# Kernel optimization log

Measured on AMD Instinct MI355X. Metric: run time of the kernel, lower is better.

Reference implementation:

```python
import jax, jax.numpy as jnp
import numpy as np

D_OUT = 32
INPUT_LEN = 2048
NUM_EIGH = 32
K_U = 3
K_Y = 2


def _top_hankel_eigh(n, k):
    # Hankel matrix Z[i,j] = 2 / ((i+j)^3 - (i+j)) for i,j in 1..n
    i = np.arange(1, n + 1, dtype=np.float64)
    s = i[:, None] + i[None, :]
    Z = 2.0 / (s ** 3 - s)
    vals, vecs = np.linalg.eigh(Z)
    return (jnp.asarray(vals[-k:], dtype=jnp.float32),
            jnp.asarray(vecs[:, -k:], dtype=jnp.float32))


def setup_inputs() -> dict:
    key = jax.random.key(0)
    k1, k2, k3, k4 = jax.random.split(key, 4)
    B = 32
    inputs = jax.random.normal(k1, (B, INPUT_LEN, D_OUT), dtype=jnp.float32)
    eig_vals, eig_vecs = _top_hankel_eigh(INPUT_LEN, NUM_EIGH)
    m_u = jax.random.normal(k2, (D_OUT, D_OUT, K_U), dtype=jnp.float32) * 0.02
    m_phi = jax.random.normal(k3, (D_OUT * NUM_EIGH, D_OUT), dtype=jnp.float32) * 0.02
    m_y = jax.random.normal(k4, (D_OUT, K_Y, D_OUT), dtype=jnp.float32) * 0.02
    return {"inputs": inputs, "eig_vals": eig_vals, "eig_vecs": eig_vecs,
            "m_u": m_u, "m_phi": m_phi, "m_y": m_y}


def _spectral_conv(v, u):
    # Causal FFT convolution of each filter v[:,k] with each channel u[:,:,d].
    # v: (l, k), u: (b, l, d) -> (b, l, k, d)
    l = v.shape[0]
    n = 2 * l
    V = jnp.fft.rfft(v, n=n, axis=0)          # (nf, k)
    U = jnp.fft.rfft(u, n=n, axis=1)          # (b, nf, d)
    P = V[None, :, :, None] * U[:, :, None, :]  # (b, nf, k, d)
    return jnp.fft.irfft(P, n=n, axis=1)[:, :l]


def _compute_x_tilde(inputs, eig_vals, eig_vecs):
    b, l, d = inputs.shape
    x_tilde = _spectral_conv(eig_vecs, inputs)                  # (b, l, k, d)
    x_tilde = x_tilde * (eig_vals ** 0.25)[None, None, :, None]
    return x_tilde.reshape(b, l, -1)                            # (b, l, k*d)


def _compute_ar_x_preds(w, x):
    # w: (d_out, d_in, k), x: (b, l, d_in) -> (b, l, d_out)
    d_out, d_in, k = w.shape
    b, l, _ = x.shape
    o = jnp.einsum('oik,bli->bklo', w, x)                       # (b, k, l, d_out)
    shifts = jnp.arange(k)
    rolled = jax.vmap(lambda oi, s: jnp.roll(oi, s, axis=1),
                      in_axes=(1, 0), out_axes=1)(o, shifts)    # (b, k, l, d_out)
    mask = (jnp.arange(l)[None, :] >= shifts[:, None]).astype(x.dtype)  # (k, l)
    return jnp.sum(rolled * mask[None, :, :, None], axis=1)


def _compute_y_t(m_y, deltas):
    # m_y: (d_out, k_y, d_out), deltas: (b, l, d_out)
    # y_t = sum_{j<k_y} m_y[:, j] @ y_{t-1-j} + delta_t
    b, l, d = deltas.shape
    ky = m_y.shape[1]
    carry0 = jnp.zeros((b, ky, d), dtype=deltas.dtype)

    def step(carry, x):
        out = jnp.einsum('oki,bki->bo', m_y, carry) + x
        carry = jnp.roll(carry, 1, axis=1).at[:, 0].set(out)
        return carry, out

    _, ys = jax.lax.scan(step, carry0, jnp.swapaxes(deltas, 0, 1))
    return jnp.swapaxes(ys, 0, 1)


def reference(inputs, eig_vals, eig_vecs, m_u, m_phi, m_y):
    x_tilde = _compute_x_tilde(inputs, eig_vals, eig_vecs)
    delta_phi = x_tilde @ m_phi
    delta_ar_u = _compute_ar_x_preds(m_u, inputs)
    return _compute_y_t(m_y, delta_phi + delta_ar_u)
```

## Files before the change

kernel.cpp:

```cpp
#include <hip/hip_runtime.h>
#include <math.h>

#define L     2048
#define NFFT  4096
#define NH    2049
#define UST   2052
#define D     32
#define B     32
#define KU    3
#define CCH   64
#define NCH   32

__device__ __forceinline__ int PHY(int i) { return i + (i >> 5); }
__device__ __forceinline__ int REV4(int i) {
  int r2 = __brev(i) >> 20;
  return ((r2 & 0x555) << 1) | ((r2 >> 1) & 0x555);
}

__device__ void dif6(float* sre, float* sim, const float2* __restrict__ tw, int tid) {
  #pragma unroll
  for (int st = 0; st < 6; ++st) {
    const int shift = 10 - 2 * st;
    const int q = 1 << shift;
    const int r = 1 << (2 * st);
    #pragma unroll
    for (int h = 0; h < 2; ++h) {
      const int idx = tid + h * 512;
      const int j = idx & (q - 1);
      const int g = idx >> shift;
      const int i0 = (g << (shift + 2)) + j;
      const int p0 = PHY(i0), p1 = PHY(i0 + q), p2 = PHY(i0 + 2 * q), p3 = PHY(i0 + 3 * q);
      float ax = sre[p0], ay = sim[p0], bx = sre[p1], by = sim[p1];
      float cx = sre[p2], cy = sim[p2], dx = sre[p3], dy = sim[p3];
      float t0x = ax + cx, t0y = ay + cy, t1x = ax - cx, t1y = ay - cy;
      float t2x = bx + dx, t2y = by + dy, t3x = bx - dx, t3y = by - dy;
      float2 w1 = tw[j * r];
      float w2x = w1.x * w1.x - w1.y * w1.y, w2y = 2.f * w1.x * w1.y;
      float w3x = w2x * w1.x - w2y * w1.y, w3y = w2x * w1.y + w2y * w1.x;
      sre[p0] = t0x + t2x; sim[p0] = t0y + t2y;
      float u1x = t1x + t3y, u1y = t1y - t3x;
      sre[p1] = u1x * w1.x - u1y * w1.y; sim[p1] = u1x * w1.y + u1y * w1.x;
      float u2x = t0x - t2x, u2y = t0y - t2y;
      sre[p2] = u2x * w2x - u2y * w2y; sim[p2] = u2x * w2y + u2y * w2x;
      float u3x = t1x - t3y, u3y = t1y + t3x;
      sre[p3] = u3x * w3x - u3y * w3y; sim[p3] = u3x * w3y + u3y * w3x;
    }
    __syncthreads();
  }
}

__device__ void dit6(float* sre, float* sim, const float2* __restrict__ tw, int tid) {
  #pragma unroll
  for (int st = 0; st < 6; ++st) {
    const int shift = 2 * st;
    const int q = 1 << shift;
    const int r = 1 << (10 - 2 * st);
    #pragma unroll
    for (int h = 0; h < 2; ++h) {
      const int idx = tid + h * 512;
      const int j = idx & (q - 1);
      const int g = idx >> shift;
      const int i0 = (g << (shift + 2)) + j;
      const int p0 = PHY(i0), p1 = PHY(i0 + q), p2 = PHY(i0 + 2 * q), p3 = PHY(i0 + 3 * q);
      float ax = sre[p0], ay = sim[p0], bx = sre[p1], by = sim[p1];
      float cx = sre[p2], cy = sim[p2], dx = sre[p3], dy = sim[p3];
      float2 w1 = tw[j * r]; w1.y = -w1.y;
      float w2x = w1.x * w1.x - w1.y * w1.y, w2y = 2.f * w1.x * w1.y;
      float w3x = w2x * w1.x - w2y * w1.y, w3y = w2x * w1.y + w2y * w1.x;
      float bpx = bx * w1.x - by * w1.y, bpy = bx * w1.y + by * w1.x;
      float cpx = cx * w2x - cy * w2y,   cpy = cx * w2y + cy * w2x;
      float dpx = dx * w3x - dy * w3y,   dpy = dx * w3y + dy * w3x;
      float t0x = ax + cpx, t0y = ay + cpy, t1x = ax - cpx, t1y = ay - cpy;
      float t2x = bpx + dpx, t2y = bpy + dpy, t3x = bpx - dpx, t3y = bpy - dpy;
      sre[p0] = t0x + t2x; sim[p0] = t0y + t2y;
      sre[p1] = t1x - t3y; sim[p1] = t1y + t3x;
      sre[p2] = t0x - t2x; sim[p2] = t0y - t2y;
      sre[p3] = t1x + t3y; sim[p3] = t1y - t3x;
    }
    __syncthreads();
  }
}

__global__ __launch_bounds__(256) void k_tr(const float* __restrict__ u,
                                            float2* __restrict__ uTp,
                                            float2* __restrict__ tw) {
  const int bx = blockIdx.x;
  const int b = blockIdx.y;
  const int tid = threadIdx.x;
  if (bx >= L / 64) {
    if (b == 0) {
      for (int jj = tid; jj < 2048; jj += 256) {
        int j = (bx - L / 64) * 2048 + jj;
        double ang = -2.0 * 3.14159265358979323846 * (double)j / (double)NFFT;
        tw[j] = make_float2((float)cos(ang), (float)sin(ang));
      }
    }
    return;
  }
  __shared__ float tile[64][33];
  const int t0 = bx * 64;
  for (int i = tid; i < 64 * 32; i += 256) {
    int tl = i >> 5, d = i & 31;
    tile[tl][d] = u[((size_t)b * L + t0 + tl) * D + d];
  }
  __syncthreads();
  for (int i = tid; i < 16 * 64; i += 256) {
    int p = i >> 6, tt = i & 63;
    uTp[((size_t)b * 16 + p) * L + t0 + tt] =
        make_float2(tile[tt][2 * p], tile[tt][2 * p + 1]);
  }
}

__global__ __launch_bounds__(512) void k_fft_fwd(const float2* __restrict__ uTp,
                                                 const float* __restrict__ eig_vecs,
                                                 const float* __restrict__ eig_vals,
                                                 const float2* __restrict__ tw,
                                                 float2* __restrict__ Ubuf,
                                                 float2* __restrict__ Vf) {
  __shared__ float sre[4224];
  __shared__ float sim[4224];
  const int blk = blockIdx.x;
  const int tid = threadIdx.x;
  if (blk < 512) {
    const float2* zp = uTp + (size_t)blk * L;
    for (int t = tid; t < L; t += 512) {
      float2 z = zp[t];
      int p = PHY(t);
      sre[p] = z.x; sim[p] = z.y;
    }
  } else {
    const int p2 = blk - 512;
    for (int t = tid; t < L; t += 512) {
      int p = PHY(t);
      sre[p] = eig_vecs[(size_t)t * D + 2 * p2];
      sim[p] = eig_vecs[(size_t)t * D + 2 * p2 + 1];
    }
  }
  for (int t = L + tid; t < NFFT; t += 512) {
    int p = PHY(t);
    sre[p] = 0.f; sim[p] = 0.f;
  }
  __syncthreads();
  dif6(sre, sim, tw, tid);
  if (blk < 512) {
    float2* r0 = Ubuf + (size_t)(2 * blk) * UST;
    float2* r1 = r0 + UST;
    for (int f = tid; f <= 2048; f += 512) {
      int pa = PHY(REV4(f));
      int pc = PHY(REV4((NFFT - f) & (NFFT - 1)));
      float Ax = sre[pa], Ay = sim[pa];
      float Bx = sre[pc], By = -sim[pc];
      r0[f] = make_float2(0.5f * (Ax + Bx), 0.5f * (Ay + By));
      float Dx = Ax - Bx, Dy = Ay - By;
      r1[f] = make_float2(0.5f * Dy, -0.5f * Dx);
    }
  } else {
    const int p2 = blk - 512;
    const float sc0 = powf(eig_vals[2 * p2], 0.25f);
    const float sc1 = powf(eig_vals[2 * p2 + 1], 0.25f);
    float2* r0 = Vf + (size_t)(2 * p2) * UST;
    float2* r1 = r0 + UST;
    for (int f = tid; f <= 2048; f += 512) {
      int pa = PHY(REV4(f));
      int pc = PHY(REV4((NFFT - f) & (NFFT - 1)));
      float Ax = sre[pa], Ay = sim[pa];
      float Bx = sre[pc], By = -sim[pc];
      r0[f] = make_float2(0.5f * sc0 * (Ax + Bx), 0.5f * sc0 * (Ay + By));
      float Dx = Ax - Bx, Dy = Ay - By;
      r1[f] = make_float2(0.5f * sc1 * Dy, -0.5f * sc1 * Dx);
    }
  }
}

#define KWFT 8
__global__ __launch_bounds__(256) void k_w(const float2* __restrict__ Vf,
                                           const float* __restrict__ m_phi,
                                           float2* __restrict__ Wm) {
  __shared__ float2 Vl[D][KWFT];
  __shared__ float  Ml[D][256];
  const int f0 = blockIdx.x * KWFT;
  const int tid = threadIdx.x;
  {
    int k = tid >> 3, ff = tid & 7;
    int f = f0 + ff;
    Vl[k][ff] = (f < NH) ? Vf[(size_t)k * UST + f] : make_float2(0.f, 0.f);
  }
  for (int c = 0; c < 4; ++c) {
    __syncthreads();
    for (int i = tid; i < D * 256; i += 256) {
      int k = i >> 8, doo = i & 255;
      Ml[k][doo] = m_phi[(size_t)k * D * D + c * 256 + doo];
    }
    __syncthreads();
    float m[D];
    #pragma unroll
    for (int k = 0; k < D; ++k) m[k] = Ml[k][tid];
    const int d = c * 8 + (tid >> 5), o = tid & 31;
    #pragma unroll
    for (int ff = 0; ff < KWFT; ++ff) {
      int f = f0 + ff;
      if (f >= NH) break;
      float2 acc = make_float2(0.f, 0.f);
      #pragma unroll
      for (int k = 0; k < D; ++k) {
        float2 v = Vl[k][ff];
        acc.x += v.x * m[k];
        acc.y += v.y * m[k];
      }
      Wm[(size_t)f * D * D + d * D + o] = acc;
    }
  }
}

#define FT 8
#define BC 8
__global__ __launch_bounds__(256) void k_mix(const float2* __restrict__ Ubuf,
                                             const float2* __restrict__ Wm,
                                             float2* __restrict__ Qbuf) {
  __shared__ float2 Ul[BC][D][FT];
  __shared__ float2 Qs[BC][D][FT];
  const int f0 = blockIdx.x * FT;
  const int bbase = blockIdx.y * 16;
  const int tid = threadIdx.x;
  const int o = tid & 31, fi = tid >> 5;
  const int f = f0 + fi;
  float2 Wr[D];
  if (f < NH) {
    const float2* wp = Wm + (size_t)f * D * D + o;
    #pragma unroll
    for (int d = 0; d < D; ++d) Wr[d] = wp[d * D];
  } else {
    #pragma unroll
    for (int d = 0; d < D; ++d) Wr[d] = make_float2(0.f, 0.f);
  }
  const int lf = tid & 7, row = tid >> 3;
  for (int b0 = bbase; b0 < bbase + 16; b0 += BC) {
    __syncthreads();
    #pragma unroll
    for (int it = 0; it < 8; ++it) {
      int r = row + it * 32;
      int bc = r >> 5, d = r & 31;
      int ff = f0 + lf;
      Ul[bc][d][lf] = (ff < NH)
          ? Ubuf[((size_t)(b0 + bc) * D + d) * UST + ff]
          : make_float2(0.f, 0.f);
    }
    __syncthreads();
    #pragma unroll
    for (int bc = 0; bc < BC; ++bc) {
      float ax = 0.f, ay = 0.f;
      #pragma unroll
      for (int d = 0; d < D; ++d) {
        float2 uu = Ul[bc][d][fi];
        float2 ww = Wr[d];
        ax += uu.x * ww.x - uu.y * ww.y;
        ay += uu.x * ww.y + uu.y * ww.x;
      }
      Qs[bc][o][(fi + o) & 7] = make_float2(ax, ay);
    }
    __syncthreads();
    #pragma unroll
    for (int it = 0; it < 8; ++it) {
      int r = row + it * 32;
      int bc = r >> 5, oo = r & 31;
      int ff = f0 + lf;
      if (ff < NH)
        Qbuf[((size_t)(b0 + bc) * D + oo) * UST + ff] = Qs[bc][oo][(lf + oo) & 7];
    }
  }
}

__global__ __launch_bounds__(512) void k_ifft(const float2* __restrict__ Qbuf,
                                              const float2* __restrict__ tw,
                                              float* __restrict__ dT) {
  __shared__ float sre[4224];
  __shared__ float sim[4224];
  const int blk = blockIdx.x;
  const int tid = threadIdx.x;
  const float2* r0 = Qbuf + (size_t)(2 * blk) * UST;
  const float2* r1 = r0 + UST;
  for (int f = tid; f <= 2048; f += 512) {
    float2 q1 = r0[f], q2 = r1[f];
    int pa = PHY(REV4(f));
    int pc = PHY(REV4((NFFT - f) & (NFFT - 1)));
    sre[pa] = q1.x - q2.y; sim[pa] = q1.y + q2.x;
    sre[pc] = q1.x + q2.y; sim[pc] = -q1.y + q2.x;
  }
  __syncthreads();
  dit6(sre, sim, tw, tid);
  float* d0 = dT + (size_t)(2 * blk) * L;
  float* d1 = d0 + L;
  const float inv = 1.0f / (float)NFFT;
  for (int t = tid; t < L; t += 512) {
    int p = PHY(t);
    d0[t] = sre[p] * inv;
    d1[t] = sim[p] * inv;
  }
}

#define TT 64
__global__ __launch_bounds__(256) void k_ar(const float* __restrict__ dT,
                                            const float* __restrict__ u,
                                            const float* __restrict__ m_u,
                                            float* __restrict__ delta) {
  __shared__ float Ds[D][TT + 1];
  __shared__ float Us[TT + 2][D];
  __shared__ float Mt[KU][D][D];
  const int b = blockIdx.y;
  const int t0 = blockIdx.x * TT;
  const int tid = threadIdx.x;
  for (int idx = tid; idx < D * D * KU; idx += blockDim.x) {
    int k = idx % KU, i = (idx / KU) % D, o = idx / (KU * D);
    Mt[k][i][o] = m_u[idx];
  }
  for (int idx = tid; idx < D * TT; idx += blockDim.x) {
    int o = idx >> 6, tt = idx & 63;
    Ds[o][tt] = dT[((size_t)b * D + o) * L + t0 + tt];
  }
  for (int idx = tid; idx < (TT + 2) * D; idx += blockDim.x) {
    int j = idx >> 5, i = idx & 31;
    int t = t0 - 2 + j;
    Us[j][i] = (t >= 0) ? u[((size_t)b * L + t) * D + i] : 0.f;
  }
  __syncthreads();
  const int o = tid & 31, ts = tid >> 5;
  for (int tt = ts; tt < TT; tt += 8) {
    int t = t0 + tt;
    float acc = Ds[o][tt];
    #pragma unroll
    for (int k2 = 0; k2 < KU; ++k2) {
      if (t >= k2) {
        const float* ur = Us[tt + 2 - k2];
        #pragma unroll
        for (int i = 0; i < D; ++i) acc += Mt[k2][i][o] * ur[i];
      }
    }
    delta[((size_t)b * L + t) * D + o] = acc;
  }
}

__global__ __launch_bounds__(1024) void k_tc(const float* __restrict__ m_y,
                                             float* __restrict__ Tc) {
  __shared__ float A[64][68];
  __shared__ float Bb[64][68];
  const int tid = threadIdx.x;
  for (int idx = tid; idx < 64 * 64; idx += blockDim.x) {
    int r = idx >> 6, c = idx & 63;
    float v;
    if (r < 32) v = m_y[(r * 2 + (c >> 5)) * D + (c & 31)];
    else        v = (c == r - 32) ? 1.f : 0.f;
    A[r][c] = v;
  }
  __syncthreads();
  const int r = tid >> 4, cg = tid & 15;
  for (int it = 0; it < 6; ++it) {
    float4 acc = make_float4(0.f, 0.f, 0.f, 0.f);
    for (int i = 0; i < 64; ++i) {
      float a = A[r][i];
      float4 v = *(const float4*)&A[i][cg * 4];
      acc.x += a * v.x; acc.y += a * v.y; acc.z += a * v.z; acc.w += a * v.w;
    }
    __syncthreads();
    *(float4*)&Bb[r][cg * 4] = acc;
    __syncthreads();
    *(float4*)&A[r][cg * 4] = *(const float4*)&Bb[r][cg * 4];
    __syncthreads();
  }
  for (int idx = tid; idx < 64 * 64; idx += blockDim.x)
    Tc[idx] = A[idx >> 6][idx & 63];
}

__global__ void k_scanA(const float* __restrict__ delta,
                        const float* __restrict__ m_y,
                        float* __restrict__ shat) {
  __shared__ float yb[2][D];
  __shared__ float Dl[CCH][D + 1];
  const int b = blockIdx.y, c = blockIdx.x;
  const int lane = threadIdx.x;
  const int o = lane & 31, h = lane >> 5;
  float m0[16], m1[16];
  #pragma unroll
  for (int i = 0; i < 16; ++i) {
    m0[i] = m_y[(o * 2 + 0) * D + h * 16 + i];
    m1[i] = m_y[(o * 2 + 1) * D + h * 16 + i];
  }
  const float* dp = delta + ((size_t)b * L + c * CCH) * D;
  for (int j = lane; j < CCH * D / 4; j += 64) {
    float4 v = ((const float4*)dp)[j];
    int base = j * 4;
    int r = base >> 5, col = base & 31;
    Dl[r][col] = v.x; Dl[r][col + 1] = v.y;
    Dl[r][col + 2] = v.z; Dl[r][col + 3] = v.w;
  }
  if (lane < D) { yb[0][lane] = 0.f; yb[1][lane] = 0.f; }
  __syncthreads();
  float ylast = 0.f, yprev = 0.f;
  for (int r = 0; r < CCH; ++r) {
    const float* y1 = yb[(r + 1) & 1];
    const float* y2 = yb[r & 1];
    float acc = 0.f;
    #pragma unroll
    for (int i = 0; i < 16; ++i)
      acc += m0[i] * y1[h * 16 + i] + m1[i] * y2[h * 16 + i];
    acc += __shfl_xor(acc, 32);
    float y = acc + Dl[r][o];
    __syncthreads();
    if (h == 0) yb[r & 1][o] = y;
    __syncthreads();
    yprev = ylast; ylast = y;
  }
  if (h == 0) {
    float* sp = shat + ((size_t)b * NCH + c) * 64;
    sp[o] = ylast;
    sp[32 + o] = yprev;
  }
}

__global__ void k_scanB(const float* __restrict__ Tc,
                        const float* __restrict__ shat,
                        float* __restrict__ sin_) {
  __shared__ float TcT[64][65];
  __shared__ float sb[64];
  const int b = blockIdx.x;
  const int r = threadIdx.x;
  for (int idx = r; idx < 64 * 64; idx += 64) {
    int rr = idx >> 6, cc = idx & 63;
    TcT[cc][rr] = Tc[idx];
  }
  sb[r] = 0.f;
  __syncthreads();
  for (int c = 0; c < NCH; ++c) {
    sin_[((size_t)b * NCH + c) * 64 + r] = sb[r];
    float acc = 0.f;
    #pragma unroll 8
    for (int i = 0; i < 64; ++i) acc += TcT[i][r] * sb[i];
    acc += shat[((size_t)b * NCH + c) * 64 + r];
    __syncthreads();
    sb[r] = acc;
    __syncthreads();
  }
}

__global__ void k_scanC(const float* __restrict__ delta,
                        const float* __restrict__ m_y,
                        const float* __restrict__ sin_,
                        float* __restrict__ out) {
  __shared__ float yb[2][D];
  __shared__ float Dl[CCH][D + 1];
  const int b = blockIdx.y, c = blockIdx.x;
  const int lane = threadIdx.x;
  const int o = lane & 31, h = lane >> 5;
  float m0[16], m1[16];
  #pragma unroll
  for (int i = 0; i < 16; ++i) {
    m0[i] = m_y[(o * 2 + 0) * D + h * 16 + i];
    m1[i] = m_y[(o * 2 + 1) * D + h * 16 + i];
  }
  const float* dp = delta + ((size_t)b * L + c * CCH) * D;
  for (int j = lane; j < CCH * D / 4; j += 64) {
    float4 v = ((const float4*)dp)[j];
    int base = j * 4;
    int r = base >> 5, col = base & 31;
    Dl[r][col] = v.x; Dl[r][col + 1] = v.y;
    Dl[r][col + 2] = v.z; Dl[r][col + 3] = v.w;
  }
  const float* sp = sin_ + ((size_t)b * NCH + c) * 64;
  if (lane < 32) yb[1][lane] = sp[lane];
  else           yb[0][lane - 32] = sp[lane];
  __syncthreads();
  float* op = out + ((size_t)b * L + c * CCH) * D;
  for (int r = 0; r < CCH; ++r) {
    const float* y1 = yb[(r + 1) & 1];
    const float* y2 = yb[r & 1];
    float acc = 0.f;
    #pragma unroll
    for (int i = 0; i < 16; ++i)
      acc += m0[i] * y1[h * 16 + i] + m1[i] * y2[h * 16 + i];
    acc += __shfl_xor(acc, 32);
    float y = acc + Dl[r][o];
    __syncthreads();
    if (h == 0) { yb[r & 1][o] = y; op[r * D + o] = y; }
    __syncthreads();
  }
}

extern "C" void kernel_launch(void* const* d_in, const int* in_sizes, int n_in,
                              void* d_out, int out_size, void* d_ws, size_t ws_size,
                              hipStream_t stream) {
  const float* u        = (const float*)d_in[0];
  const float* eig_vals = (const float*)d_in[1];
  const float* eig_vecs = (const float*)d_in[2];
  const float* m_u      = (const float*)d_in[3];
  const float* m_phi    = (const float*)d_in[4];
  const float* m_y      = (const float*)d_in[5];
  float* out = (float*)d_out;

  char* ws = (char*)d_ws;
  size_t off = 0;
  auto alloc = [&](size_t bytes) -> void* {
    void* p = ws + off;
    off += bytes;
    off = (off + 255) & ~(size_t)255;
    return p;
  };
  float2* tw   = (float2*)alloc((size_t)NFFT * sizeof(float2));
  float2* uTp  = (float2*)alloc((size_t)B * 16 * L * sizeof(float2));
  float2* Vf   = (float2*)alloc((size_t)D * UST * sizeof(float2));
  float2* Wm   = (float2*)alloc((size_t)NH * D * D * sizeof(float2));
  float2* Ubuf = (float2*)alloc((size_t)B * D * UST * sizeof(float2));
  float2* Qbuf = (float2*)alloc((size_t)B * D * UST * sizeof(float2));
  float*  Tc   = (float*)alloc(64 * 64 * sizeof(float));
  float*  shat = (float*)alloc((size_t)B * NCH * 64 * sizeof(float));
  float*  sinb = (float*)alloc((size_t)B * NCH * 64 * sizeof(float));
  float* dT    = (float*)uTp;
  float* delta = (float*)Ubuf;

  k_tr     <<<dim3(L / 64 + 2, B), 256, 0, stream>>>(u, uTp, tw);
  k_fft_fwd<<<528, 512, 0, stream>>>(uTp, eig_vecs, eig_vals, tw, Ubuf, Vf);
  k_w      <<<(NH + KWFT - 1) / KWFT, 256, 0, stream>>>(Vf, m_phi, Wm);
  k_mix    <<<dim3((NH + FT - 1) / FT, 2), 256, 0, stream>>>(Ubuf, Wm, Qbuf);
  k_ifft   <<<B * 16, 512, 0, stream>>>(Qbuf, tw, dT);
  k_ar     <<<dim3(L / TT, B), 256, 0, stream>>>(dT, u, m_u, delta);
  k_tc     <<<1, 1024, 0, stream>>>(m_y, Tc);
  k_scanA  <<<dim3(NCH, B), 64, 0, stream>>>(delta, m_y, shat);
  k_scanB  <<<B, 64, 0, stream>>>(Tc, shat, sinb);
  k_scanC  <<<dim3(NCH, B), 64, 0, stream>>>(delta, m_y, sinb, out);
}
```

Measured before the change: 265.0 us.

## Fuse AR, scan stages and Tc into cooperative kernel; compute twiddles inline

Removes the transpose kernel by having the forward FFT read strided channel pairs directly from the input, and replaces the twiddle table with on-the-fly __sincosf. The Tc matrix-power computation is folded into an extra block of k_w. The AR prediction and the three scan phases are merged into one cooperative kernel that uses grid-wide syncs instead of separate launches. This cuts launch count and intermediate delta traffic, but adds grid.sync overhead, uses a single block per batch for the serial chunk-carry phase, and lowers twiddle precision.

```diff
diff --git a/kernel.cpp b/kernel.cpp
--- a/kernel.cpp
+++ b/kernel.cpp
@@ -1,5 +1,8 @@
 #include <hip/hip_runtime.h>
+#include <hip/hip_cooperative_groups.h>
 #include <math.h>
+
+namespace cg = cooperative_groups;
 
 #define L     2048
 #define NFFT  4096
@@ -16,8 +19,15 @@
   int r2 = __brev(i) >> 20;
   return ((r2 & 0x555) << 1) | ((r2 >> 1) & 0x555);
 }
-
-__device__ void dif6(float* sre, float* sim, const float2* __restrict__ tw, int tid) {
+template<int SGN>
+__device__ __forceinline__ float2 twid(int jr) {
+  float th = (float)jr * 1.5339807878856412e-3f;
+  float s, c;
+  __sincosf(th, &s, &c);
+  return make_float2(c, SGN > 0 ? -s : s);
+}
+
+__device__ void dif6(float* sre, float* sim, int tid) {
   #pragma unroll
   for (int st = 0; st < 6; ++st) {
     const int shift = 10 - 2 * st;
@@ -34,7 +44,7 @@
       float cx = sre[p2], cy = sim[p2], dx = sre[p3], dy = sim[p3];
       float t0x = ax + cx, t0y = ay + cy, t1x = ax - cx, t1y = ay - cy;
       float t2x = bx + dx, t2y = by + dy, t3x = bx - dx, t3y = by - dy;
-      float2 w1 = tw[j * r];
+      float2 w1 = twid<1>(j * r);
       float w2x = w1.x * w1.x - w1.y * w1.y, w2y = 2.f * w1.x * w1.y;
       float w3x = w2x * w1.x - w2y * w1.y, w3y = w2x * w1.y + w2y * w1.x;
       sre[p0] = t0x + t2x; sim[p0] = t0y + t2y;
@@ -49,7 +59,7 @@
   }
 }
 
-__device__ void dit6(float* sre, float* sim, const float2* __restrict__ tw, int tid) {
+__device__ void dit6(float* sre, float* sim, int tid) {
   #pragma unroll
   for (int st = 0; st < 6; ++st) {
     const int shift = 2 * st;
@@ -64,7 +74,7 @@
       const int p0 = PHY(i0), p1 = PHY(i0 + q), p2 = PHY(i0 + 2 * q), p3 = PHY(i0 + 3 * q);
       float ax = sre[p0], ay = sim[p0], bx = sre[p1], by = sim[p1];
       float cx = sre[p2], cy = sim[p2], dx = sre[p3], dy = sim[p3];
-      float2 w1 = tw[j * r]; w1.y = -w1.y;
+      float2 w1 = twid<-1>(j * r);
       float w2x = w1.x * w1.x - w1.y * w1.y, w2y = 2.f * w1.x * w1.y;
       float w3x = w2x * w1.x - w2y * w1.y, w3y = w2x * w1.y + w2y * w1.x;
       float bpx = bx * w1.x - by * w1.y, bpy = bx * w1.y + by * w1.x;
@@ -81,40 +91,9 @@
   }
 }
 
-__global__ __launch_bounds__(256) void k_tr(const float* __restrict__ u,
-                                            float2* __restrict__ uTp,
-                                            float2* __restrict__ tw) {
-  const int bx = blockIdx.x;
-  const int b = blockIdx.y;
-  const int tid = threadIdx.x;
-  if (bx >= L / 64) {
-    if (b == 0) {
-      for (int jj = tid; jj < 2048; jj += 256) {
-        int j = (bx - L / 64) * 2048 + jj;
-        double ang = -2.0 * 3.14159265358979323846 * (double)j / (double)NFFT;
-        tw[j] = make_float2((float)cos(ang), (float)sin(ang));
-      }
-    }
-    return;
-  }
-  __shared__ float tile[64][33];
-  const int t0 = bx * 64;
-  for (int i = tid; i < 64 * 32; i += 256) {
-    int tl = i >> 5, d = i & 31;
-    tile[tl][d] = u[((size_t)b * L + t0 + tl) * D + d];
-  }
-  __syncthreads();
-  for (int i = tid; i < 16 * 64; i += 256) {
-    int p = i >> 6, tt = i & 63;
-    uTp[((size_t)b * 16 + p) * L + t0 + tt] =
-        make_float2(tile[tt][2 * p], tile[tt][2 * p + 1]);
-  }
-}
-
-__global__ __launch_bounds__(512) void k_fft_fwd(const float2* __restrict__ uTp,
+__global__ __launch_bounds__(512) void k_fft_fwd(const float* __restrict__ u,
                                                  const float* __restrict__ eig_vecs,
                                                  const float* __restrict__ eig_vals,
-                                                 const float2* __restrict__ tw,
                                                  float2* __restrict__ Ubuf,
                                                  float2* __restrict__ Vf) {
   __shared__ float sre[4224];
@@ -122,28 +101,30 @@
   const int blk = blockIdx.x;
   const int tid = threadIdx.x;
   if (blk < 512) {
-    const float2* zp = uTp + (size_t)blk * L;
+    const int p = blk >> 5, b = blk & 31;
+    const float* up = u + (size_t)b * L * D + 2 * p;
     for (int t = tid; t < L; t += 512) {
-      float2 z = zp[t];
-      int p = PHY(t);
-      sre[p] = z.x; sim[p] = z.y;
+      float2 z = *(const float2*)(up + (size_t)t * D);
+      int pp = PHY(t);
+      sre[pp] = z.x; sim[pp] = z.y;
     }
   } else {
     const int p2 = blk - 512;
     for (int t = tid; t < L; t += 512) {
-      int p = PHY(t);
-      sre[p] = eig_vecs[(size_t)t * D + 2 * p2];
-      sim[p] = eig_vecs[(size_t)t * D + 2 * p2 + 1];
+      int pp = PHY(t);
+      sre[pp] = eig_vecs[(size_t)t * D + 2 * p2];
+      sim[pp] = eig_vecs[(size_t)t * D + 2 * p2 + 1];
     }
   }
   for (int t = L + tid; t < NFFT; t += 512) {
-    int p = PHY(t);
-    sre[p] = 0.f; sim[p] = 0.f;
+    int pp = PHY(t);
+    sre[pp] = 0.f; sim[pp] = 0.f;
   }
   __syncthreads();
-  dif6(sre, sim, tw, tid);
+  dif6(sre, sim, tid);
   if (blk < 512) {
-    float2* r0 = Ubuf + (size_t)(2 * blk) * UST;
+    const int p = blk >> 5, b = blk & 31;
+    float2* r0 = Ubuf + (size_t)(b * 32 + 2 * p) * UST;
     float2* r1 = r0 + UST;
     for (int f = tid; f <= 2048; f += 512) {
       int pa = PHY(REV4(f));
@@ -175,11 +156,46 @@
 #define KWFT 8
 __global__ __launch_bounds__(256) void k_w(const float2* __restrict__ Vf,
                                            const float* __restrict__ m_phi,
-                                           float2* __restrict__ Wm) {
+                                           const float* __restrict__ m_y,
+                                           float2* __restrict__ Wm,
+                                           float* __restrict__ Tc) {
+  __shared__ float smem[8704];
   __shared__ float2 Vl[D][KWFT];
-  __shared__ float  Ml[D][256];
+  const int tid = threadIdx.x;
+  if (blockIdx.x == (NH + KWFT - 1) / KWFT) {
+    float* A  = smem;
+    float* Bb = smem + 4352;
+    for (int idx = tid; idx < 64 * 64; idx += 256) {
+      int r = idx >> 6, cc = idx & 63;
+      float v;
+      if (r < 32) v = m_y[(r * 2 + (cc >> 5)) * D + (cc & 31)];
+      else        v = (cc == r - 32) ? 1.f : 0.f;
+      A[r * 68 + cc] = v;
+    }
+    __syncthreads();
+    const int r = tid >> 2, c0 = (tid & 3) << 4;
+    for (int it = 0; it < 6; ++it) {
+      float acc[16];
+      #pragma unroll
+      for (int j2 = 0; j2 < 16; ++j2) acc[j2] = 0.f;
+      for (int i = 0; i < 64; ++i) {
+        float a = A[r * 68 + i];
+        #pragma unroll
+        for (int j2 = 0; j2 < 16; ++j2) acc[j2] += a * A[i * 68 + c0 + j2];
+      }
+      __syncthreads();
+      #pragma unroll
+      for (int j2 = 0; j2 < 16; ++j2) Bb[r * 68 + c0 + j2] = acc[j2];
+      __syncthreads();
+      #pragma unroll
+      for (int j2 = 0; j2 < 16; ++j2) A[r * 68 + c0 + j2] = Bb[r * 68 + c0 + j2];
+      __syncthreads();
+    }
+    for (int idx = tid; idx < 64 * 64; idx += 256)
+      Tc[idx] = A[(idx >> 6) * 68 + (idx & 63)];
+    return;
+  }
   const int f0 = blockIdx.x * KWFT;
-  const int tid = threadIdx.x;
   {
     int k = tid >> 3, ff = tid & 7;
     int f = f0 + ff;
@@ -187,14 +203,12 @@
   }
   for (int c = 0; c < 4; ++c) {
     __syncthreads();
-    for (int i = tid; i < D * 256; i += 256) {
-      int k = i >> 8, doo = i & 255;
-      Ml[k][doo] = m_phi[(size_t)k * D * D + c * 256 + doo];
-    }
+    for (int i = tid; i < D * 256; i += 256)
+      smem[i] = m_phi[(size_t)(i >> 8) * D * D + c * 256 + (i & 255)];
     __syncthreads();
     float m[D];
     #pragma unroll
-    for (int k = 0; k < D; ++k) m[k] = Ml[k][tid];
+    for (int k = 0; k < D; ++k) m[k] = smem[k * 256 + tid];
     const int d = c * 8 + (tid >> 5), o = tid & 31;
     #pragma unroll
     for (int ff = 0; ff < KWFT; ++ff) {
@@ -271,7 +285,6 @@
 }
 
 __global__ __launch_bounds__(512) void k_ifft(const float2* __restrict__ Qbuf,
-                                              const float2* __restrict__ tw,
                                               float* __restrict__ dT) {
   __shared__ float sre[4224];
   __shared__ float sim[4224];
@@ -287,110 +300,68 @@
     sre[pc] = q1.x + q2.y; sim[pc] = -q1.y + q2.x;
   }
   __syncthreads();
-  dit6(sre, sim, tw, tid);
+  dit6(sre, sim, tid);
   float* d0 = dT + (size_t)(2 * blk) * L;
   float* d1 = d0 + L;
   const float inv = 1.0f / (float)NFFT;
   for (int t = tid; t < L; t += 512) {
-    int p = PHY(t);
-    d0[t] = sre[p] * inv;
-    d1[t] = sim[p] * inv;
-  }
-}
-
-#define TT 64
-__global__ __launch_bounds__(256) void k_ar(const float* __restrict__ dT,
-                                            const float* __restrict__ u,
-                                            const float* __restrict__ m_u,
-                                            float* __restrict__ delta) {
-  __shared__ float Ds[D][TT + 1];
-  __shared__ float Us[TT + 2][D];
-  __shared__ float Mt[KU][D][D];
-  const int b = blockIdx.y;
-  const int t0 = blockIdx.x * TT;
-  const int tid = threadIdx.x;
-  for (int idx = tid; idx < D * D * KU; idx += blockDim.x) {
-    int k = idx % KU, i = (idx / KU) % D, o = idx / (KU * D);
-    Mt[k][i][o] = m_u[idx];
-  }
-  for (int idx = tid; idx < D * TT; idx += blockDim.x) {
-    int o = idx >> 6, tt = idx & 63;
-    Ds[o][tt] = dT[((size_t)b * D + o) * L + t0 + tt];
-  }
-  for (int idx = tid; idx < (TT + 2) * D; idx += blockDim.x) {
-    int j = idx >> 5, i = idx & 31;
-    int t = t0 - 2 + j;
-    Us[j][i] = (t >= 0) ? u[((size_t)b * L + t) * D + i] : 0.f;
-  }
-  __syncthreads();
-  const int o = tid & 31, ts = tid >> 5;
-  for (int tt = ts; tt < TT; tt += 8) {
-    int t = t0 + tt;
-    float acc = Ds[o][tt];
-    #pragma unroll
-    for (int k2 = 0; k2 < KU; ++k2) {
-      if (t >= k2) {
-        const float* ur = Us[tt + 2 - k2];
-        #pragma unroll
-        for (int i = 0; i < D; ++i) acc += Mt[k2][i][o] * ur[i];
-      }
-    }
-    delta[((size_t)b * L + t) * D + o] = acc;
-  }
-}
-
-__global__ __launch_bounds__(1024) void k_tc(const float* __restrict__ m_y,
-                                             float* __restrict__ Tc) {
-  __shared__ float A[64][68];
-  __shared__ float Bb[64][68];
-  const int tid = threadIdx.x;
-  for (int idx = tid; idx < 64 * 64; idx += blockDim.x) {
-    int r = idx >> 6, c = idx & 63;
-    float v;
-    if (r < 32) v = m_y[(r * 2 + (c >> 5)) * D + (c & 31)];
-    else        v = (c == r - 32) ? 1.f : 0.f;
-    A[r][c] = v;
-  }
-  __syncthreads();
-  const int r = tid >> 4, cg = tid & 15;
-  for (int it = 0; it < 6; ++it) {
-    float4 acc = make_float4(0.f, 0.f, 0.f, 0.f);
-    for (int i = 0; i < 64; ++i) {
-      float a = A[r][i];
-      float4 v = *(const float4*)&A[i][cg * 4];
-      acc.x += a * v.x; acc.y += a * v.y; acc.z += a * v.z; acc.w += a * v.w;
-    }
-    __syncthreads();
-    *(float4*)&Bb[r][cg * 4] = acc;
-    __syncthreads();
-    *(float4*)&A[r][cg * 4] = *(const float4*)&Bb[r][cg * 4];
-    __syncthreads();
-  }
-  for (int idx = tid; idx < 64 * 64; idx += blockDim.x)
-    Tc[idx] = A[idx >> 6][idx & 63];
-}
-
-__global__ void k_scanA(const float* __restrict__ delta,
-                        const float* __restrict__ m_y,
-                        float* __restrict__ shat) {
+    int pp = PHY(t);
+    d0[t] = sre[pp] * inv;
+    d1[t] = sim[pp] * inv;
+  }
+}
+
+__global__ __launch_bounds__(64) void k_scan(const float* __restrict__ dT,
+                                             const float* __restrict__ u,
+                                             const float* __restrict__ m_u,
+                                             const float* __restrict__ m_y,
+                                             const float* __restrict__ Tc,
+                                             float* __restrict__ shat,
+                                             float* __restrict__ sinb,
+                                             float* __restrict__ out) {
+  __shared__ float Dl[CCH][D + 1];
+  __shared__ float ovl[4224];
   __shared__ float yb[2][D];
-  __shared__ float Dl[CCH][D + 1];
-  const int b = blockIdx.y, c = blockIdx.x;
-  const int lane = threadIdx.x;
-  const int o = lane & 31, h = lane >> 5;
+  cg::grid_group grid = cg::this_grid();
+  const int c = blockIdx.x, b = blockIdx.y;
+  const int lane = threadIdx.x, o = lane & 31, h = lane >> 5;
+  const int t0 = c * CCH;
   float m0[16], m1[16];
   #pragma unroll
   for (int i = 0; i < 16; ++i) {
     m0[i] = m_y[(o * 2 + 0) * D + h * 16 + i];
     m1[i] = m_y[(o * 2 + 1) * D + h * 16 + i];
   }
-  const float* dp = delta + ((size_t)b * L + c * CCH) * D;
-  for (int j = lane; j < CCH * D / 4; j += 64) {
-    float4 v = ((const float4*)dp)[j];
-    int base = j * 4;
-    int r = base >> 5, col = base & 31;
-    Dl[r][col] = v.x; Dl[r][col + 1] = v.y;
-    Dl[r][col + 2] = v.z; Dl[r][col + 3] = v.w;
+  float mu[KU][16];
+  #pragma unroll
+  for (int kk = 0; kk < KU; ++kk)
+    #pragma unroll
+    for (int i = 0; i < 16; ++i)
+      mu[kk][i] = m_u[(size_t)(o * D + h * 16 + i) * KU + kk];
+  for (int idx = lane; idx < D * CCH; idx += 64) {
+    int oo = idx >> 6, tt = idx & 63;
+    Dl[tt][oo] = dT[((size_t)b * D + oo) * L + t0 + tt];
+  }
+  float* Us = ovl;
+  for (int idx = lane; idx < (CCH + 2) * D; idx += 64) {
+    int j = idx >> 5, i = idx & 31;
+    int t = t0 - 2 + j;
+    Us[j * D + i] = (t >= 0) ? u[((size_t)b * L + t) * D + i] : 0.f;
+  }
+  __syncthreads();
+  for (int tt = 0; tt < CCH; ++tt) {
+    int t = t0 + tt;
+    float acc = 0.f;
+    #pragma unroll
+    for (int kk = 0; kk < KU; ++kk) {
+      if (t >= kk) {
+        const float* ur = Us + (tt + 2 - kk) * D + h * 16;
+        #pragma unroll
+        for (int i = 0; i < 16; ++i) acc += mu[kk][i] * ur[i];
+      }
+    }
+    acc += __shfl_xor(acc, 32);
+    if (h == 0) Dl[tt][o] += acc;
   }
   if (lane < D) { yb[0][lane] = 0.f; yb[1][lane] = 0.f; }
   __syncthreads();
@@ -414,73 +385,47 @@
     sp[o] = ylast;
     sp[32 + o] = yprev;
   }
-}
-
-__global__ void k_scanB(const float* __restrict__ Tc,
-                        const float* __restrict__ shat,
-                        float* __restrict__ sin_) {
-  __shared__ float TcT[64][65];
-  __shared__ float sb[64];
-  const int b = blockIdx.x;
-  const int r = threadIdx.x;
-  for (int idx = r; idx < 64 * 64; idx += 64) {
-    int rr = idx >> 6, cc = idx & 63;
-    TcT[cc][rr] = Tc[idx];
-  }
-  sb[r] = 0.f;
-  __syncthreads();
-  for (int c = 0; c < NCH; ++c) {
-    sin_[((size_t)b * NCH + c) * 64 + r] = sb[r];
-    float acc = 0.f;
-    #pragma unroll 8
-    for (int i = 0; i < 64; ++i) acc += TcT[i][r] * sb[i];
-    acc += shat[((size_t)b * NCH + c) * 64 + r];
-    __syncthreads();
-    sb[r] = acc;
-    __syncthreads();
-  }
-}
-
-__global__ void k_scanC(const float* __restrict__ delta,
-                        const float* __restrict__ m_y,
-                        const float* __restrict__ sin_,
-                        float* __restrict__ out) {
-  __shared__ float yb[2][D];
-  __shared__ float Dl[CCH][D + 1];
-  const int b = blockIdx.y, c = blockIdx.x;
-  const int lane = threadIdx.x;
-  const int o = lane & 31, h = lane >> 5;
-  float m0[16], m1[16];
-  #pragma unroll
-  for (int i = 0; i < 16; ++i) {
-    m0[i] = m_y[(o * 2 + 0) * D + h * 16 + i];
-    m1[i] = m_y[(o * 2 + 1) * D + h * 16 + i];
-  }
-  const float* dp = delta + ((size_t)b * L + c * CCH) * D;
-  for (int j = lane; j < CCH * D / 4; j += 64) {
-    float4 v = ((const float4*)dp)[j];
-    int base = j * 4;
-    int r = base >> 5, col = base & 31;
-    Dl[r][col] = v.x; Dl[r][col + 1] = v.y;
-    Dl[r][col + 2] = v.z; Dl[r][col + 3] = v.w;
-  }
-  const float* sp = sin_ + ((size_t)b * NCH + c) * 64;
-  if (lane < 32) yb[1][lane] = sp[lane];
-  else           yb[0][lane - 32] = sp[lane];
-  __syncthreads();
-  float* op = out + ((size_t)b * L + c * CCH) * D;
-  for (int r = 0; r < CCH; ++r) {
-    const float* y1 = yb[(r + 1) & 1];
-    const float* y2 = yb[r & 1];
-    float acc = 0.f;
-    #pragma unroll
-    for (int i = 0; i < 16; ++i)
-      acc += m0[i] * y1[h * 16 + i] + m1[i] * y2[h * 16 + i];
-    acc += __shfl_xor(acc, 32);
-    float y = acc + Dl[r][o];
-    __syncthreads();
-    if (h == 0) { yb[r & 1][o] = y; op[r * D + o] = y; }
-    __syncthreads();
+  grid.sync();
+  if (c == 0) {
+    float* TcT = ovl;
+    float* sb  = ovl + 64 * 65;
+    for (int idx = lane; idx < 64 * 64; idx += 64) {
+      int rr = idx >> 6, cc2 = idx & 63;
+      TcT[cc2 * 65 + rr] = Tc[idx];
+    }
+    sb[lane] = 0.f;
+    __syncthreads();
+    for (int ch = 0; ch < NCH; ++ch) {
+      sinb[((size_t)b * NCH + ch) * 64 + lane] = sb[lane];
+      float acc = 0.f;
+      #pragma unroll 8
+      for (int i = 0; i < 64; ++i) acc += TcT[i * 65 + lane] * sb[i];
+      acc += shat[((size_t)b * NCH + ch) * 64 + lane];
+      __syncthreads();
+      sb[lane] = acc;
+      __syncthreads();
+    }
+  }
+  grid.sync();
+  {
+    const float* sp = sinb + ((size_t)b * NCH + c) * 64;
+    if (lane < 32) yb[1][lane] = sp[lane];
+    else           yb[0][lane - 32] = sp[lane];
+    __syncthreads();
+    float* op = out + ((size_t)b * L + t0) * D;
+    for (int r = 0; r < CCH; ++r) {
+      const float* y1 = yb[(r + 1) & 1];
+      const float* y2 = yb[r & 1];
+      float acc = 0.f;
+      #pragma unroll
+      for (int i = 0; i < 16; ++i)
+        acc += m0[i] * y1[h * 16 + i] + m1[i] * y2[h * 16 + i];
+      acc += __shfl_xor(acc, 32);
+      float y = acc + Dl[r][o];
+      __syncthreads();
+      if (h == 0) { yb[r & 1][o] = y; op[r * D + o] = y; }
+      __syncthreads();
+    }
   }
 }
 
@@ -503,26 +448,22 @@
     off = (off + 255) & ~(size_t)255;
     return p;
   };
-  float2* tw   = (float2*)alloc((size_t)NFFT * sizeof(float2));
-  float2* uTp  = (float2*)alloc((size_t)B * 16 * L * sizeof(float2));
   float2* Vf   = (float2*)alloc((size_t)D * UST * sizeof(float2));
   float2* Wm   = (float2*)alloc((size_t)NH * D * D * sizeof(float2));
   float2* Ubuf = (float2*)alloc((size_t)B * D * UST * sizeof(float2));
   float2* Qbuf = (float2*)alloc((size_t)B * D * UST * sizeof(float2));
+  float*  dT   = (float*)alloc((size_t)B * D * L * sizeof(float));
   float*  Tc   = (float*)alloc(64 * 64 * sizeof(float));
   float*  shat = (float*)alloc((size_t)B * NCH * 64 * sizeof(float));
   float*  sinb = (float*)alloc((size_t)B * NCH * 64 * sizeof(float));
-  float* dT    = (float*)uTp;
-  float* delta = (float*)Ubuf;
-
-  k_tr     <<<dim3(L / 64 + 2, B), 256, 0, stream>>>(u, uTp, tw);
-  k_fft_fwd<<<528, 512, 0, stream>>>(uTp, eig_vecs, eig_vals, tw, Ubuf, Vf);
-  k_w      <<<(NH + KWFT - 1) / KWFT, 256, 0, stream>>>(Vf, m_phi, Wm);
+
+  k_fft_fwd<<<528, 512, 0, stream>>>(u, eig_vecs, eig_vals, Ubuf, Vf);
+  k_w      <<<(NH + KWFT - 1) / KWFT + 1, 256, 0, stream>>>(Vf, m_phi, m_y, Wm, Tc);
   k_mix    <<<dim3((NH + FT - 1) / FT, 2), 256, 0, stream>>>(Ubuf, Wm, Qbuf);
-  k_ifft   <<<B * 16, 512, 0, stream>>>(Qbuf, tw, dT);
-  k_ar     <<<dim3(L / TT, B), 256, 0, stream>>>(dT, u, m_u, delta);
-  k_tc     <<<1, 1024, 0, stream>>>(m_y, Tc);
-  k_scanA  <<<dim3(NCH, B), 64, 0, stream>>>(delta, m_y, shat);
-  k_scanB  <<<B, 64, 0, stream>>>(Tc, shat, sinb);
-  k_scanC  <<<dim3(NCH, B), 64, 0, stream>>>(delta, m_y, sinb, out);
-}
+  k_ifft   <<<B * 16, 512, 0, stream>>>(Qbuf, dT);
+
+  void* args[] = { (void*)&dT, (void*)&u, (void*)&m_u, (void*)&m_y,
+                   (void*)&Tc, (void*)&shat, (void*)&sinb, (void*)&out };
+  hipLaunchCooperativeKernel((const void*)k_scan, dim3(NCH, B), dim3(64),
+                             args, 0, stream);
+}
```

Result: slower. 413.0 us (+55.8%).
